# Kernel optimization log

Hardware: AMD Instinct MI355X
Metric: run time of the kernel (lower is better)

Reference implementation:

```python
import jax, jax.numpy as jnp
import numpy as np

POS_RATIO = 0.5
EPS = 1e-6


def setup_inputs() -> dict:
    key = jax.random.key(0)
    k1, k2, k3, k4 = jax.random.split(key, 4)
    N, C, D, H, W = 8, 256, 8, 16, 16
    q = jax.random.normal(k1, (N, C, D, H, W), dtype=jnp.float32)
    k = jax.random.normal(k2, (N, C, D, H, W), dtype=jnp.float32)
    # coords: (x0, y0, z0, x1, y1, z1) with lower-right > upper-left
    uq = jax.random.uniform(k3, (N, 3), dtype=jnp.float32) * 0.5
    uk = jax.random.uniform(k4, (N, 3), dtype=jnp.float32) * 0.5
    coord_q = jnp.concatenate([uq, uq + 0.5], axis=1)
    coord_k = jnp.concatenate([uk, uk + 0.5], axis=1)
    return {"q": q, "k": k, "coord_q": coord_q, "coord_k": coord_k}


def _centers(coord, D, H, W):
    """Per-batch voxel-center coordinates. coord: [N,6]. Returns cx, cy, cz each [N, D*H*W], plus bin diag [N]."""
    bw = (coord[:, 3] - coord[:, 0]) / W  # [N]
    bh = (coord[:, 4] - coord[:, 1]) / H
    bd = (coord[:, 5] - coord[:, 2]) / D
    gz, gy, gx = jnp.meshgrid(jnp.arange(D, dtype=coord.dtype),
                              jnp.arange(H, dtype=coord.dtype),
                              jnp.arange(W, dtype=coord.dtype), indexing="ij")
    gx = (gx + 0.5).reshape(-1)[None, :]  # [1, DHW]
    gy = (gy + 0.5).reshape(-1)[None, :]
    gz = (gz + 0.5).reshape(-1)[None, :]
    cx = gx * bw[:, None] + coord[:, 0][:, None]
    cy = gy * bh[:, None] + coord[:, 1][:, None]
    cz = gz * bd[:, None] + coord[:, 2][:, None]
    diag = jnp.sqrt(bw ** 2 + bh ** 2 + bd ** 2)  # [N]
    return cx, cy, cz, diag


def reference(q, k, coord_q, coord_k):
    N, C, D, H, W = q.shape
    qf = q.reshape(N, C, -1)  # [N, C, P], P = D*H*W
    kf = k.reshape(N, C, -1)
    cqx, cqy, cqz, q_diag = _centers(coord_q, D, H, W)
    ckx, cky, ckz, k_diag = _centers(coord_k, D, H, W)
    max_diag = jnp.maximum(q_diag, k_diag)  # [N]
    # pairwise center distance, normalized by max bin diagonal: [N, P, P]
    dist = jnp.sqrt((cqx[:, :, None] - ckx[:, None, :]) ** 2
                    + (cqy[:, :, None] - cky[:, None, :]) ** 2
                    + (cqz[:, :, None] - ckz[:, None, :]) ** 2) / max_diag[:, None, None]
    pos_mask = jax.lax.stop_gradient((dist < POS_RATIO).astype(q.dtype))
    # logit[n, p, p'] = sum_c q[n,c,p] * k[n,c,p']
    logit = jnp.einsum("ncp,ncq->npq", qf, kf)
    loss = (logit * pos_mask).sum((-2, -1)) / (pos_mask.sum((-2, -1)) + EPS)  # [N]
    return -2.0 * loss.mean()
```

## Files before the change

### kernel.cpp

```cpp
#include <hip/hip_runtime.h>
#include <cstdint>
#include <cstddef>

#define NB 8
#define CH 256
#define DD 8
#define HH 16
#define WW 16
#define PP 2048
#define MAXL 32

#define OFF_LIST  65536
#define OFF_PART  1114112

__device__ __forceinline__ int z_window(float czq, float bdk, float k2, float maxd) {
    float lim = 0.500060f * maxd;
    int zk0 = -1;
    #pragma unroll
    for (int zk = 0; zk < DD; ++zk) {
        float czk = __fadd_rn(__fmul_rn(__fadd_rn((float)zk, 0.5f), bdk), k2);
        bool feas = fabsf(__fsub_rn(czq, czk)) < lim;
        if (feas && zk0 < 0) zk0 = zk;
    }
    if (zk0 > DD - 2) zk0 = DD - 2;
    return zk0;
}

__global__ __launch_bounds__(256) void mask_kernel(
    const float* __restrict__ coord_q, const float* __restrict__ coord_k,
    int* __restrict__ counts, unsigned short* __restrict__ lists)
{
    int wave = blockIdx.x * 4 + (threadIdx.x >> 6);
    int lane = threadIdx.x & 63;
    int n = wave >> 11;
    int p = wave & (PP - 1);

    const float* cq = coord_q + n * 6;
    const float* ck = coord_k + n * 6;
    float q0 = cq[0], q1 = cq[1], q2 = cq[2];
    float bwq = __fdiv_rn(__fsub_rn(cq[3], q0), (float)WW);
    float bhq = __fdiv_rn(__fsub_rn(cq[4], q1), (float)HH);
    float bdq = __fdiv_rn(__fsub_rn(cq[5], q2), (float)DD);
    float k0 = ck[0], k1 = ck[1], k2 = ck[2];
    float bwk = __fdiv_rn(__fsub_rn(ck[3], k0), (float)WW);
    float bhk = __fdiv_rn(__fsub_rn(ck[4], k1), (float)HH);
    float bdk = __fdiv_rn(__fsub_rn(ck[5], k2), (float)DD);

    float diagq = __fsqrt_rn(__fadd_rn(__fadd_rn(__fmul_rn(bwq, bwq), __fmul_rn(bhq, bhq)),
                                       __fmul_rn(bdq, bdq)));
    float diagk = __fsqrt_rn(__fadd_rn(__fadd_rn(__fmul_rn(bwk, bwk), __fmul_rn(bhk, bhk)),
                                       __fmul_rn(bdk, bdk)));
    float maxd = fmaxf(diagq, diagk);

    int ix = p & 15, iy = (p >> 4) & 15, iz = p >> 8;
    float cqx = __fadd_rn(__fmul_rn(__fadd_rn((float)ix, 0.5f), bwq), q0);
    float cqy = __fadd_rn(__fmul_rn(__fadd_rn((float)iy, 0.5f), bhq), q1);
    float cqz = __fadd_rn(__fmul_rn(__fadd_rn((float)iz, 0.5f), bdq), q2);

    int zk0 = z_window(cqz, bdk, k2, maxd);
    if (zk0 < 0) {
        if (lane == 0) counts[n * PP + p] = 0;
        return;
    }
    int base_p = zk0 << 8;

    float half_maxd = 0.5f * maxd;
    float thr2 = half_maxd * half_maxd * 1.001f;

    int count = 0;
    for (int it = 0; it < 8; ++it) {
        int pp = base_p + ((it << 6) | lane);
        int jx = pp & 15, jy = (pp >> 4) & 15, jz = pp >> 8;
        float ckx = __fadd_rn(__fmul_rn(__fadd_rn((float)jx, 0.5f), bwk), k0);
        float cky = __fadd_rn(__fmul_rn(__fadd_rn((float)jy, 0.5f), bhk), k1);
        float ckz = __fadd_rn(__fmul_rn(__fadd_rn((float)jz, 0.5f), bdk), k2);
        float dx = __fsub_rn(cqx, ckx);
        float dy = __fsub_rn(cqy, cky);
        float dz = __fsub_rn(cqz, ckz);
        float d2 = __fadd_rn(__fadd_rn(__fmul_rn(dx, dx), __fmul_rn(dy, dy)),
                             __fmul_rn(dz, dz));
        bool pos = false;
        if (d2 < thr2) {
            float dist = __fdiv_rn(__fsqrt_rn(d2), maxd);
            pos = dist < 0.5f;
        }
        unsigned long long m = __ballot(pos);
        if (pos) {
            int pref = __popcll(m & ((1ull << lane) - 1ull));
            int j = count + pref;
            if (j < MAXL)
                lists[((size_t)(n * MAXL + j)) * PP + p] = (unsigned short)pp;
        }
        count += (int)__popcll(m);
    }
    if (lane == 0)
        counts[n * PP + p] = count;
}

#define CC 8
__global__ __launch_bounds__(256) void dot_kernel(
    const float* __restrict__ q, const float* __restrict__ k,
    const float* __restrict__ coord_q, const float* __restrict__ coord_k,
    const int* __restrict__ counts, const unsigned short* __restrict__ lists,
    float* __restrict__ partial)
{
    __shared__ float klds[CC][512];
    __shared__ float red[256];

    int t  = threadIdx.x;
    int cg = blockIdx.x;
    int zq = blockIdx.y;
    int n  = blockIdx.z;
    int flat = (n * 8 + zq) * 32 + cg;
    int c0 = cg * CC;

    const float* cq = coord_q + n * 6;
    const float* ck = coord_k + n * 6;
    float q2 = cq[2], k2 = ck[2];
    float bwq = __fdiv_rn(__fsub_rn(cq[3], cq[0]), (float)WW);
    float bhq = __fdiv_rn(__fsub_rn(cq[4], cq[1]), (float)HH);
    float bdq = __fdiv_rn(__fsub_rn(cq[5], q2), (float)DD);
    float bwk = __fdiv_rn(__fsub_rn(ck[3], ck[0]), (float)WW);
    float bhk = __fdiv_rn(__fsub_rn(ck[4], ck[1]), (float)HH);
    float bdk = __fdiv_rn(__fsub_rn(ck[5], k2), (float)DD);
    float diagq = __fsqrt_rn(__fadd_rn(__fadd_rn(__fmul_rn(bwq, bwq), __fmul_rn(bhq, bhq)),
                                       __fmul_rn(bdq, bdq)));
    float diagk = __fsqrt_rn(__fadd_rn(__fadd_rn(__fmul_rn(bwk, bwk), __fmul_rn(bhk, bhk)),
                                       __fmul_rn(bdk, bdk)));
    float maxd = fmaxf(diagq, diagk);
    float cqz = __fadd_rn(__fmul_rn(__fadd_rn((float)zq, 0.5f), bdq), q2);

    int zk0 = z_window(cqz, bdk, k2, maxd);
    if (zk0 < 0) {
        if (t == 0) partial[flat] = 0.0f;
        return;
    }
    int base_p = zk0 << 8;

    {
        const float* ksrc = k + ((size_t)(n * CH + c0)) * PP + base_p;
        #pragma unroll
        for (int i = 0; i < 4; ++i) {
            int f = i * 256 + t;
            int c = f >> 7;
            int u = (f & 127) << 2;
            float4 v = *(const float4*)(ksrc + (size_t)c * PP + u);
            klds[c][u + 0] = v.x;
            klds[c][u + 1] = v.y;
            klds[c][u + 2] = v.z;
            klds[c][u + 3] = v.w;
        }
    }
    __syncthreads();

    int p = (zq << 8) + t;
    int cnt = counts[n * PP + p];
    cnt = cnt < MAXL ? cnt : MAXL;

    float s[CC];
    #pragma unroll
    for (int c = 0; c < CC; ++c) s[c] = 0.0f;

    const unsigned short* lp = lists + (size_t)n * MAXL * PP + p;
    int idx = (cnt > 0) ? ((int)lp[0] - base_p) : 0;
    for (int j = 0; j < cnt; ++j) {
        int nidx = (j + 1 < cnt) ? ((int)lp[(size_t)(j + 1) * PP] - base_p) : 0;
        #pragma unroll
        for (int c = 0; c < CC; ++c)
            s[c] += klds[c][idx];
        idx = nidx;
    }

    float acc = 0.0f;
    const float* qcol = q + ((size_t)(n * CH + c0)) * PP + p;
    #pragma unroll
    for (int c = 0; c < CC; ++c)
        acc += qcol[(size_t)c * PP] * s[c];

    red[t] = acc;
    __syncthreads();
    for (int off = 128; off > 0; off >>= 1) {
        if (t < off) red[t] += red[t + off];
        __syncthreads();
    }
    if (t == 0) partial[flat] = red[0];
}

__global__ __launch_bounds__(512) void final_kernel(const float* __restrict__ partial,
                                                    const int* __restrict__ counts,
                                                    float* __restrict__ out)
{
    __shared__ float numsh[NB];
    __shared__ float densh[NB];
    int t = threadIdx.x;
    int n = t >> 6, lane = t & 63;

    float sp = 0.0f;
    for (int i = 0; i < 256 / 64; ++i)
        sp += partial[n * 256 + i * 64 + lane];
    int sc = 0;
    for (int i = 0; i < PP / 64; ++i)
        sc += counts[n * PP + i * 64 + lane];
    for (int off = 32; off > 0; off >>= 1) {
        sp += __shfl_down(sp, off, 64);
        sc += __shfl_down(sc, off, 64);
    }
    if (lane == 0) { numsh[n] = sp; densh[n] = (float)sc; }
    __syncthreads();
    if (t == 0) {
        float r = 0.0f;
        for (int i = 0; i < NB; ++i)
            r += numsh[i] / (densh[i] + 1e-6f);
        out[0] = -2.0f * (r / (float)NB);
    }
}

extern "C" void kernel_launch(void* const* d_in, const int* in_sizes, int n_in,
                              void* d_out, int out_size, void* d_ws, size_t ws_size,
                              hipStream_t stream) {
    const float* q       = (const float*)d_in[0];
    const float* k       = (const float*)d_in[1];
    const float* coord_q = (const float*)d_in[2];
    const float* coord_k = (const float*)d_in[3];
    float* out = (float*)d_out;

    char* w = (char*)d_ws;
    int* counts           = (int*)w;
    unsigned short* lists = (unsigned short*)(w + OFF_LIST);
    float* partial        = (float*)(w + OFF_PART);

    mask_kernel<<<(NB * PP) / 4, 256, 0, stream>>>(coord_q, coord_k, counts, lists);
    dot_kernel<<<dim3(CH / CC, DD, NB), 256, 0, stream>>>(q, k, coord_q, coord_k,
                                                          counts, lists, partial);
    final_kernel<<<1, 512, 0, stream>>>(partial, counts, out);
}
```

Measured before the change: 88.18 us.

## Fuse mask computation into dot kernel with bounded x/y neighbor window

Removes the separate mask kernel and the per-voxel neighbor lists in global memory. Each thread of the dot kernel now recomputes its positive-mask neighbors directly, enumerating only a bounded x/y window over the two candidate z slices and accumulating from the LDS-staged k tile. Mask counts are reduced in the same block and written as per-(n,z) partial denominators, so the final kernel reads far less data. This trades one launch and the list writes and reads for redundant mask arithmetic repeated across all 32 channel-group blocks, plus divergent loops.

```diff
diff --git a/kernel.cpp b/kernel.cpp
--- a/kernel.cpp
+++ b/kernel.cpp
@@ -8,10 +8,8 @@
 #define HH 16
 #define WW 16
 #define PP 2048
-#define MAXL 32
-
-#define OFF_LIST  65536
-#define OFF_PART  1114112
+
+#define OFF_DPART 8192
 
 __device__ __forceinline__ int z_window(float czq, float bdk, float k2, float maxd) {
     float lim = 0.500060f * maxd;
@@ -26,86 +24,15 @@
     return zk0;
 }
 
-__global__ __launch_bounds__(256) void mask_kernel(
-    const float* __restrict__ coord_q, const float* __restrict__ coord_k,
-    int* __restrict__ counts, unsigned short* __restrict__ lists)
-{
-    int wave = blockIdx.x * 4 + (threadIdx.x >> 6);
-    int lane = threadIdx.x & 63;
-    int n = wave >> 11;
-    int p = wave & (PP - 1);
-
-    const float* cq = coord_q + n * 6;
-    const float* ck = coord_k + n * 6;
-    float q0 = cq[0], q1 = cq[1], q2 = cq[2];
-    float bwq = __fdiv_rn(__fsub_rn(cq[3], q0), (float)WW);
-    float bhq = __fdiv_rn(__fsub_rn(cq[4], q1), (float)HH);
-    float bdq = __fdiv_rn(__fsub_rn(cq[5], q2), (float)DD);
-    float k0 = ck[0], k1 = ck[1], k2 = ck[2];
-    float bwk = __fdiv_rn(__fsub_rn(ck[3], k0), (float)WW);
-    float bhk = __fdiv_rn(__fsub_rn(ck[4], k1), (float)HH);
-    float bdk = __fdiv_rn(__fsub_rn(ck[5], k2), (float)DD);
-
-    float diagq = __fsqrt_rn(__fadd_rn(__fadd_rn(__fmul_rn(bwq, bwq), __fmul_rn(bhq, bhq)),
-                                       __fmul_rn(bdq, bdq)));
-    float diagk = __fsqrt_rn(__fadd_rn(__fadd_rn(__fmul_rn(bwk, bwk), __fmul_rn(bhk, bhk)),
-                                       __fmul_rn(bdk, bdk)));
-    float maxd = fmaxf(diagq, diagk);
-
-    int ix = p & 15, iy = (p >> 4) & 15, iz = p >> 8;
-    float cqx = __fadd_rn(__fmul_rn(__fadd_rn((float)ix, 0.5f), bwq), q0);
-    float cqy = __fadd_rn(__fmul_rn(__fadd_rn((float)iy, 0.5f), bhq), q1);
-    float cqz = __fadd_rn(__fmul_rn(__fadd_rn((float)iz, 0.5f), bdq), q2);
-
-    int zk0 = z_window(cqz, bdk, k2, maxd);
-    if (zk0 < 0) {
-        if (lane == 0) counts[n * PP + p] = 0;
-        return;
-    }
-    int base_p = zk0 << 8;
-
-    float half_maxd = 0.5f * maxd;
-    float thr2 = half_maxd * half_maxd * 1.001f;
-
-    int count = 0;
-    for (int it = 0; it < 8; ++it) {
-        int pp = base_p + ((it << 6) | lane);
-        int jx = pp & 15, jy = (pp >> 4) & 15, jz = pp >> 8;
-        float ckx = __fadd_rn(__fmul_rn(__fadd_rn((float)jx, 0.5f), bwk), k0);
-        float cky = __fadd_rn(__fmul_rn(__fadd_rn((float)jy, 0.5f), bhk), k1);
-        float ckz = __fadd_rn(__fmul_rn(__fadd_rn((float)jz, 0.5f), bdk), k2);
-        float dx = __fsub_rn(cqx, ckx);
-        float dy = __fsub_rn(cqy, cky);
-        float dz = __fsub_rn(cqz, ckz);
-        float d2 = __fadd_rn(__fadd_rn(__fmul_rn(dx, dx), __fmul_rn(dy, dy)),
-                             __fmul_rn(dz, dz));
-        bool pos = false;
-        if (d2 < thr2) {
-            float dist = __fdiv_rn(__fsqrt_rn(d2), maxd);
-            pos = dist < 0.5f;
-        }
-        unsigned long long m = __ballot(pos);
-        if (pos) {
-            int pref = __popcll(m & ((1ull << lane) - 1ull));
-            int j = count + pref;
-            if (j < MAXL)
-                lists[((size_t)(n * MAXL + j)) * PP + p] = (unsigned short)pp;
-        }
-        count += (int)__popcll(m);
-    }
-    if (lane == 0)
-        counts[n * PP + p] = count;
-}
-
 #define CC 8
-__global__ __launch_bounds__(256) void dot_kernel(
+__global__ __launch_bounds__(256) void fused_kernel(
     const float* __restrict__ q, const float* __restrict__ k,
     const float* __restrict__ coord_q, const float* __restrict__ coord_k,
-    const int* __restrict__ counts, const unsigned short* __restrict__ lists,
-    float* __restrict__ partial)
+    float* __restrict__ partial, float* __restrict__ dpart)
 {
     __shared__ float klds[CC][512];
-    __shared__ float red[256];
+    __shared__ float redf[256];
+    __shared__ int   redi[256];
 
     int t  = threadIdx.x;
     int cg = blockIdx.x;
@@ -116,12 +43,13 @@
 
     const float* cq = coord_q + n * 6;
     const float* ck = coord_k + n * 6;
-    float q2 = cq[2], k2 = ck[2];
-    float bwq = __fdiv_rn(__fsub_rn(cq[3], cq[0]), (float)WW);
-    float bhq = __fdiv_rn(__fsub_rn(cq[4], cq[1]), (float)HH);
+    float q0 = cq[0], q1 = cq[1], q2 = cq[2];
+    float k0 = ck[0], k1 = ck[1], k2 = ck[2];
+    float bwq = __fdiv_rn(__fsub_rn(cq[3], q0), (float)WW);
+    float bhq = __fdiv_rn(__fsub_rn(cq[4], q1), (float)HH);
     float bdq = __fdiv_rn(__fsub_rn(cq[5], q2), (float)DD);
-    float bwk = __fdiv_rn(__fsub_rn(ck[3], ck[0]), (float)WW);
-    float bhk = __fdiv_rn(__fsub_rn(ck[4], ck[1]), (float)HH);
+    float bwk = __fdiv_rn(__fsub_rn(ck[3], k0), (float)WW);
+    float bhk = __fdiv_rn(__fsub_rn(ck[4], k1), (float)HH);
     float bdk = __fdiv_rn(__fsub_rn(ck[5], k2), (float)DD);
     float diagq = __fsqrt_rn(__fadd_rn(__fadd_rn(__fmul_rn(bwq, bwq), __fmul_rn(bhq, bhq)),
                                        __fmul_rn(bdq, bdq)));
@@ -132,7 +60,10 @@
 
     int zk0 = z_window(cqz, bdk, k2, maxd);
     if (zk0 < 0) {
-        if (t == 0) partial[flat] = 0.0f;
+        if (t == 0) {
+            partial[flat] = 0.0f;
+            if (cg == 0) dpart[n * 8 + zq] = 0.0f;
+        }
         return;
     }
     int base_p = zk0 << 8;
@@ -153,41 +84,80 @@
     }
     __syncthreads();
 
+    int ix = t & 15, iy = (t >> 4) & 15;
+    float cqx = __fadd_rn(__fmul_rn(__fadd_rn((float)ix, 0.5f), bwq), q0);
+    float cqy = __fadd_rn(__fmul_rn(__fadd_rn((float)iy, 0.5f), bhq), q1);
+
+    float lim = 0.500060f * maxd;
+    float tx = (cqx - k0) / bwk - 0.5f;
+    float ty = (cqy - k1) / bhk - 0.5f;
+    float rx = lim / bwk + 0.03f;
+    float ry = lim / bhk + 0.03f;
+    int jx0 = (int)ceilf(tx - rx);  if (jx0 < 0) jx0 = 0;
+    int jx1 = (int)floorf(tx + rx); if (jx1 > WW - 1) jx1 = WW - 1;
+    int jy0 = (int)ceilf(ty - ry);  if (jy0 < 0) jy0 = 0;
+    int jy1 = (int)floorf(ty + ry); if (jy1 > HH - 1) jy1 = HH - 1;
+
+    float half_maxd = 0.5f * maxd;
+    float thr2 = half_maxd * half_maxd * 1.001f;
+
+    float s[CC];
+    #pragma unroll
+    for (int c = 0; c < CC; ++c) s[c] = 0.0f;
+    int cnt = 0;
+
+    for (int dzI = 0; dzI < 2; ++dzI) {
+        int jz = zk0 + dzI;
+        float ckz = __fadd_rn(__fmul_rn(__fadd_rn((float)jz, 0.5f), bdk), k2);
+        float dz  = __fsub_rn(cqz, ckz);
+        float dz2 = __fmul_rn(dz, dz);
+        for (int jy = jy0; jy <= jy1; ++jy) {
+            float cky = __fadd_rn(__fmul_rn(__fadd_rn((float)jy, 0.5f), bhk), k1);
+            float dy  = __fsub_rn(cqy, cky);
+            float dy2 = __fmul_rn(dy, dy);
+            for (int jx = jx0; jx <= jx1; ++jx) {
+                float ckx = __fadd_rn(__fmul_rn(__fadd_rn((float)jx, 0.5f), bwk), k0);
+                float dx  = __fsub_rn(cqx, ckx);
+                float dx2 = __fmul_rn(dx, dx);
+                float d2  = __fadd_rn(__fadd_rn(dx2, dy2), dz2);
+                bool pos = false;
+                if (d2 < thr2) {
+                    float dist = __fdiv_rn(__fsqrt_rn(d2), maxd);
+                    pos = dist < 0.5f;
+                }
+                if (pos) {
+                    ++cnt;
+                    int idx = (dzI << 8) + (jy << 4) + jx;
+                    #pragma unroll
+                    for (int c = 0; c < CC; ++c)
+                        s[c] += klds[c][idx];
+                }
+            }
+        }
+    }
+
     int p = (zq << 8) + t;
-    int cnt = counts[n * PP + p];
-    cnt = cnt < MAXL ? cnt : MAXL;
-
-    float s[CC];
-    #pragma unroll
-    for (int c = 0; c < CC; ++c) s[c] = 0.0f;
-
-    const unsigned short* lp = lists + (size_t)n * MAXL * PP + p;
-    int idx = (cnt > 0) ? ((int)lp[0] - base_p) : 0;
-    for (int j = 0; j < cnt; ++j) {
-        int nidx = (j + 1 < cnt) ? ((int)lp[(size_t)(j + 1) * PP] - base_p) : 0;
-        #pragma unroll
-        for (int c = 0; c < CC; ++c)
-            s[c] += klds[c][idx];
-        idx = nidx;
-    }
-
     float acc = 0.0f;
     const float* qcol = q + ((size_t)(n * CH + c0)) * PP + p;
     #pragma unroll
     for (int c = 0; c < CC; ++c)
         acc += qcol[(size_t)c * PP] * s[c];
 
-    red[t] = acc;
+    redf[t] = acc;
+    redi[t] = cnt;
     __syncthreads();
     for (int off = 128; off > 0; off >>= 1) {
-        if (t < off) red[t] += red[t + off];
+        if (t < off) { redf[t] += redf[t + off]; redi[t] += redi[t + off]; }
         __syncthreads();
     }
-    if (t == 0) partial[flat] = red[0];
+    if (t == 0) {
+        partial[flat] = redf[0];
+        if (cg == 0) dpart[n * 8 + zq] = (float)redi[0];
+    }
 }
 
 __global__ __launch_bounds__(512) void final_kernel(const float* __restrict__ partial,
-                                                    const int* __restrict__ counts,
+                                                    const float* __restrict__ dpart,
                                                     float* __restrict__ out)
 {
     __shared__ float numsh[NB];
@@ -196,16 +166,15 @@
     int n = t >> 6, lane = t & 63;
 
     float sp = 0.0f;
-    for (int i = 0; i < 256 / 64; ++i)
+    #pragma unroll
+    for (int i = 0; i < 4; ++i)
         sp += partial[n * 256 + i * 64 + lane];
-    int sc = 0;
-    for (int i = 0; i < PP / 64; ++i)
-        sc += counts[n * PP + i * 64 + lane];
+    float sc = (lane < 8) ? dpart[n * 8 + lane] : 0.0f;
     for (int off = 32; off > 0; off >>= 1) {
         sp += __shfl_down(sp, off, 64);
         sc += __shfl_down(sc, off, 64);
     }
-    if (lane == 0) { numsh[n] = sp; densh[n] = (float)sc; }
+    if (lane == 0) { numsh[n] = sp; densh[n] = sc; }
     __syncthreads();
     if (t == 0) {
         float r = 0.0f;
@@ -225,12 +194,10 @@
     float* out = (float*)d_out;
 
     char* w = (char*)d_ws;
-    int* counts           = (int*)w;
-    unsigned short* lists = (unsigned short*)(w + OFF_LIST);
-    float* partial        = (float*)(w + OFF_PART);
-
-    mask_kernel<<<(NB * PP) / 4, 256, 0, stream>>>(coord_q, coord_k, counts, lists);
-    dot_kernel<<<dim3(CH / CC, DD, NB), 256, 0, stream>>>(q, k, coord_q, coord_k,
-                                                          counts, lists, partial);
-    final_kernel<<<1, 512, 0, stream>>>(partial, counts, out);
-}
+    float* partial = (float*)w;
+    float* dpart   = (float*)(w + OFF_DPART);
+
+    fused_kernel<<<dim3(CH / CC, DD, NB), 256, 0, stream>>>(q, k, coord_q, coord_k,
+                                                            partial, dpart);
+    final_kernel<<<1, 512, 0, stream>>>(partial, dpart, out);
+}
```

After: 82.57 us. -6.4%, faster.
